# Kernel tuning notes

Hardware: AMD Instinct MI355X
Metric: run time of the kernel (lower is better)

The kernel has to match this reference:

```python
import jax, jax.numpy as jnp
import numpy as np


def setup_inputs() -> dict:
    key = jax.random.key(0)
    k1, k2 = jax.random.split(key)
    N, H, K, E = 8192, 4096, 2, 64
    x = jax.random.normal(k1, (N, H), dtype=jnp.float32)
    row_idx = jnp.arange(N * K, dtype=jnp.int32).reshape(N, K)
    expert_idx = jax.random.randint(k2, (N, K), 0, E, dtype=jnp.int32)
    return {"x": x, "row_idx": row_idx, "expert_idx": expert_idx, "active_num": N * K}


def reference(x, row_idx, expert_idx, active_num):
    # x: [N, H]; row_idx, expert_idx: [N, K]
    N, H = x.shape
    K = expert_idx.shape[1]
    NK = N * K

    expert_flat = expert_idx.reshape(-1)  # [N*K]
    row_flat = row_idx.reshape(-1)        # [N*K]

    # Step 1: stable sort by expert id, carry row indices
    sorted_indices = jnp.argsort(expert_flat, stable=True)
    expanded_expert_idx = expert_flat[sorted_indices]
    dst_to_src = row_flat[sorted_indices]

    # Step 2: invert the permutation: src_to_dst[dst_to_src[i]] = i
    expanded_row_idx = jnp.zeros(NK, dtype=jnp.int32).at[dst_to_src].set(
        jnp.arange(NK, dtype=jnp.int32)
    )

    # Step 3: gather x rows; dst_to_src % N gives the original token row
    expanded_x = x[dst_to_src % N]  # [N*K, H]

    return expanded_x, expanded_row_idx, expanded_expert_idx
```

## Files before the change

kernel.cpp:

```cpp
#include <hip/hip_runtime.h>
#include <hip/hip_bf16.h>

#define TPB 256
#define NEXPERT 64

typedef float f32x4 __attribute__((ext_vector_type(4)));

__global__ void k_hist(const int* __restrict__ expert, int NK, int NB,
                       int* __restrict__ counts) {
    __shared__ int h[NEXPERT];
    const int b = blockIdx.x;
    for (int e = threadIdx.x; e < NEXPERT; e += blockDim.x) h[e] = 0;
    __syncthreads();
    const int i = b * TPB + threadIdx.x;
    if (i < NK) atomicAdd(&h[expert[i]], 1);
    __syncthreads();
    for (int e = threadIdx.x; e < NEXPERT; e += blockDim.x)
        counts[e * NB + b] = h[e];
}

__global__ void k_scan(int* __restrict__ counts, int M) {
    __shared__ int s[1024];
    const int t = threadIdx.x;
    const int nt = blockDim.x;
    const int ipt = (M + nt - 1) / nt;
    int v[8];
    int sum = 0;
    for (int j = 0; j < ipt; ++j) {
        const int idx = t * ipt + j;
        v[j] = (idx < M) ? counts[idx] : 0;
        sum += v[j];
    }
    s[t] = sum;
    __syncthreads();
    for (int off = 1; off < nt; off <<= 1) {
        const int x = (t >= off) ? s[t - off] : 0;
        __syncthreads();
        s[t] += x;
        __syncthreads();
    }
    int base = (t == 0) ? 0 : s[t - 1];
    for (int j = 0; j < ipt; ++j) {
        const int idx = t * ipt + j;
        const int c = v[j];
        if (idx < M) counts[idx] = base;
        base += c;
    }
}

__global__ void k_scatter(const int* __restrict__ expert,
                          const int* __restrict__ rowi,
                          int NK, int NB,
                          const int* __restrict__ base,
                          float* __restrict__ out_row,
                          float* __restrict__ out_expert,
                          int* __restrict__ dst_of_r) {
    __shared__ int h[TPB / 64][NEXPERT + 1];
    const int b = blockIdx.x;
    const int tid = threadIdx.x;
    const int w = tid >> 6;
    const int lane = tid & 63;
    const int i = b * TPB + tid;
    const bool valid = (i < NK);
    const int e = valid ? expert[i] : NEXPERT;

    for (int idx = tid; idx < (TPB / 64) * (NEXPERT + 1); idx += TPB)
        (&h[0][0])[idx] = 0;
    __syncthreads();

    unsigned long long mask = ~0ull;
#pragma unroll
    for (int bit = 0; bit < 7; ++bit) {
        const unsigned long long bv = __ballot((e >> bit) & 1);
        mask &= ((e >> bit) & 1) ? bv : ~bv;
    }
    const int rank_w = __popcll(mask & ((1ull << lane) - 1ull));
    const int cnt_w  = __popcll(mask);
    if (rank_w == 0) h[w][e] = cnt_w;
    __syncthreads();

    if (valid) {
        int rank = rank_w;
        for (int w2 = 0; w2 < w; ++w2) rank += h[w2][e];
        const int dst = base[e * NB + b] + rank;
        const int r = rowi[i];
        out_expert[dst] = (float)e;
        out_row[r] = (float)dst;
        dst_of_r[r] = dst;
    }
}

template <int K>
__global__ void k_gatherT(const float* __restrict__ x,
                          const int* __restrict__ dst_of_r,
                          float* __restrict__ out_x, int H, int N) {
    const int t = blockIdx.x;
    const f32x4* __restrict__ src = (const f32x4*)(x + (size_t)t * (size_t)H);
    size_t ob[K];
#pragma unroll
    for (int kk = 0; kk < K; ++kk)
        ob[kk] = (size_t)dst_of_r[t + kk * N] * (size_t)H;
    const int n4 = H >> 2;
    for (int j = threadIdx.x; j < n4; j += blockDim.x) {
        const f32x4 v = src[j];
#pragma unroll
        for (int kk = 0; kk < K; ++kk)
            __builtin_nontemporal_store(v, (f32x4*)(out_x + ob[kk]) + j);
    }
}

__global__ void k_gather_gen(const float* __restrict__ x,
                             const int* __restrict__ dst_of_r,
                             float* __restrict__ out_x, int H, int N, int K) {
    const int t = blockIdx.x;
    const f32x4* __restrict__ src = (const f32x4*)(x + (size_t)t * (size_t)H);
    const int n4 = H >> 2;
    for (int kk = 0; kk < K; ++kk) {
        const size_t ob = (size_t)dst_of_r[t + kk * N] * (size_t)H;
        for (int j = threadIdx.x; j < n4; j += blockDim.x)
            __builtin_nontemporal_store(src[j], (f32x4*)(out_x + ob) + j);
    }
}

extern "C" void kernel_launch(void* const* d_in, const int* in_sizes, int n_in,
                              void* d_out, int out_size, void* d_ws, size_t ws_size,
                              hipStream_t stream) {
    const float* x    = (const float*)d_in[0];
    const int*   rowi = (const int*)d_in[1];
    const int*   expi = (const int*)d_in[2];

    const int NK = in_sizes[1];
    const int H  = (out_size - 2 * NK) / NK;
    const int N  = in_sizes[0] / H;
    const int K  = NK / N;
    const int NB = (NK + TPB - 1) / TPB;

    float* out_x      = (float*)d_out;
    float* out_row    = out_x + (size_t)NK * (size_t)H;
    float* out_expert = out_row + NK;

    int* counts   = (int*)d_ws;
    int* dst_of_r = counts + NEXPERT * NB;

    k_hist   <<<NB, TPB, 0, stream>>>(expi, NK, NB, counts);
    k_scan   <<<1, 1024, 0, stream>>>(counts, NEXPERT * NB);
    k_scatter<<<NB, TPB, 0, stream>>>(expi, rowi, NK, NB, counts,
                                      out_row, out_expert, dst_of_r);

    switch (K) {
        case 1: k_gatherT<1><<<N, TPB, 0, stream>>>(x, dst_of_r, out_x, H, N); break;
        case 2: k_gatherT<2><<<N, TPB, 0, stream>>>(x, dst_of_r, out_x, H, N); break;
        case 3: k_gatherT<3><<<N, TPB, 0, stream>>>(x, dst_of_r, out_x, H, N); break;
        case 4: k_gatherT<4><<<N, TPB, 0, stream>>>(x, dst_of_r, out_x, H, N); break;
        default: k_gather_gen<<<N, TPB, 0, stream>>>(x, dst_of_r, out_x, H, N, K); break;
    }
}
```

Before: 77.08 us.

## Fuse histogram, scan and scatter into a single-block prelude kernel

Replaces the three-kernel counting sort (per-block histogram, global scan, scatter) with one 1024-thread single-block kernel. It computes expert counts via wave ballots, scans them with shuffles, then ranks and scatters in chunks. The gather kernel reads destination indices from the float row output instead of a separate int workspace. This removes two launches and workspace traffic, but serializes the sort onto one CU with many block barriers.

Result: slower. 100.9 us (+30.9%).

```diff
diff --git a/kernel.cpp b/kernel.cpp
--- a/kernel.cpp
+++ b/kernel.cpp
@@ -3,103 +3,99 @@
 
 #define TPB 256
 #define NEXPERT 64
+#define PRE_T 1024
+#define PRE_W (PRE_T / 64)
 
 typedef float f32x4 __attribute__((ext_vector_type(4)));
 
-__global__ void k_hist(const int* __restrict__ expert, int NK, int NB,
-                       int* __restrict__ counts) {
-    __shared__ int h[NEXPERT];
-    const int b = blockIdx.x;
-    for (int e = threadIdx.x; e < NEXPERT; e += blockDim.x) h[e] = 0;
-    __syncthreads();
-    const int i = b * TPB + threadIdx.x;
-    if (i < NK) atomicAdd(&h[expert[i]], 1);
-    __syncthreads();
-    for (int e = threadIdx.x; e < NEXPERT; e += blockDim.x)
-        counts[e * NB + b] = h[e];
-}
-
-__global__ void k_scan(int* __restrict__ counts, int M) {
-    __shared__ int s[1024];
-    const int t = threadIdx.x;
-    const int nt = blockDim.x;
-    const int ipt = (M + nt - 1) / nt;
-    int v[8];
-    int sum = 0;
-    for (int j = 0; j < ipt; ++j) {
-        const int idx = t * ipt + j;
-        v[j] = (idx < M) ? counts[idx] : 0;
-        sum += v[j];
-    }
-    s[t] = sum;
-    __syncthreads();
-    for (int off = 1; off < nt; off <<= 1) {
-        const int x = (t >= off) ? s[t - off] : 0;
-        __syncthreads();
-        s[t] += x;
-        __syncthreads();
-    }
-    int base = (t == 0) ? 0 : s[t - 1];
-    for (int j = 0; j < ipt; ++j) {
-        const int idx = t * ipt + j;
-        const int c = v[j];
-        if (idx < M) counts[idx] = base;
-        base += c;
-    }
-}
-
-__global__ void k_scatter(const int* __restrict__ expert,
-                          const int* __restrict__ rowi,
-                          int NK, int NB,
-                          const int* __restrict__ base,
-                          float* __restrict__ out_row,
-                          float* __restrict__ out_expert,
-                          int* __restrict__ dst_of_r) {
-    __shared__ int h[TPB / 64][NEXPERT + 1];
-    const int b = blockIdx.x;
+__global__ __launch_bounds__(PRE_T) void k_prelude(
+    const int* __restrict__ expert, const int* __restrict__ rowi, int NK,
+    float* __restrict__ out_row, float* __restrict__ out_expert) {
+    __shared__ int hist[NEXPERT];
+    __shared__ int wcnt[PRE_W][NEXPERT + 1];
     const int tid = threadIdx.x;
     const int w = tid >> 6;
     const int lane = tid & 63;
-    const int i = b * TPB + tid;
-    const bool valid = (i < NK);
-    const int e = valid ? expert[i] : NEXPERT;
 
-    for (int idx = tid; idx < (TPB / 64) * (NEXPERT + 1); idx += TPB)
-        (&h[0][0])[idx] = 0;
+    for (int idx = tid; idx < NEXPERT; idx += PRE_T) hist[idx] = 0;
     __syncthreads();
 
-    unsigned long long mask = ~0ull;
+    for (int base_i = 0; base_i < NK; base_i += PRE_T) {
+        const int i = base_i + tid;
+        const bool valid = (i < NK);
+        const int e = valid ? expert[i] : NEXPERT;
+        unsigned long long mask = ~0ull;
 #pragma unroll
-    for (int bit = 0; bit < 7; ++bit) {
-        const unsigned long long bv = __ballot((e >> bit) & 1);
-        mask &= ((e >> bit) & 1) ? bv : ~bv;
+        for (int bit = 0; bit < 7; ++bit) {
+            const unsigned long long bv = __ballot((e >> bit) & 1);
+            mask &= ((e >> bit) & 1) ? bv : ~bv;
+        }
+        const int rank_w = __popcll(mask & ((1ull << lane) - 1ull));
+        if (valid && rank_w == 0) atomicAdd(&hist[e], __popcll(mask));
     }
-    const int rank_w = __popcll(mask & ((1ull << lane) - 1ull));
-    const int cnt_w  = __popcll(mask);
-    if (rank_w == 0) h[w][e] = cnt_w;
     __syncthreads();
 
-    if (valid) {
-        int rank = rank_w;
-        for (int w2 = 0; w2 < w; ++w2) rank += h[w2][e];
-        const int dst = base[e * NB + b] + rank;
-        const int r = rowi[i];
-        out_expert[dst] = (float)e;
-        out_row[r] = (float)dst;
-        dst_of_r[r] = dst;
+    if (tid < NEXPERT) {
+        const int c = hist[tid];
+        int v = c;
+#pragma unroll
+        for (int off = 1; off < NEXPERT; off <<= 1) {
+            const int u = __shfl_up(v, off, 64);
+            if (lane >= off) v += u;
+        }
+        hist[tid] = v - c;
+    }
+    __syncthreads();
+
+    for (int base_i = 0; base_i < NK; base_i += PRE_T) {
+        const int i = base_i + tid;
+        const bool valid = (i < NK);
+        const int e = valid ? expert[i] : NEXPERT;
+
+        for (int idx = tid; idx < PRE_W * (NEXPERT + 1); idx += PRE_T)
+            (&wcnt[0][0])[idx] = 0;
+        __syncthreads();
+
+        unsigned long long mask = ~0ull;
+#pragma unroll
+        for (int bit = 0; bit < 7; ++bit) {
+            const unsigned long long bv = __ballot((e >> bit) & 1);
+            mask &= ((e >> bit) & 1) ? bv : ~bv;
+        }
+        const int rank_w = __popcll(mask & ((1ull << lane) - 1ull));
+        const int cnt_w  = __popcll(mask);
+        if (valid && rank_w == 0) wcnt[w][e] = cnt_w;
+        __syncthreads();
+
+        if (valid) {
+            int rank = rank_w;
+            for (int w2 = 0; w2 < w; ++w2) rank += wcnt[w2][e];
+            const int dst = hist[e] + rank;
+            const int r = rowi[i];
+            out_row[r] = (float)dst;
+            out_expert[dst] = (float)e;
+        }
+        __syncthreads();
+
+        if (tid < NEXPERT) {
+            int tot = 0;
+            for (int w2 = 0; w2 < PRE_W; ++w2) tot += wcnt[w2][tid];
+            hist[tid] += tot;
+        }
+        __syncthreads();
     }
 }
 
 template <int K>
 __global__ void k_gatherT(const float* __restrict__ x,
-                          const int* __restrict__ dst_of_r,
+                          const float* __restrict__ row_f,
                           float* __restrict__ out_x, int H, int N) {
     const int t = blockIdx.x;
     const f32x4* __restrict__ src = (const f32x4*)(x + (size_t)t * (size_t)H);
     size_t ob[K];
 #pragma unroll
     for (int kk = 0; kk < K; ++kk)
-        ob[kk] = (size_t)dst_of_r[t + kk * N] * (size_t)H;
+        ob[kk] = (size_t)(int)row_f[t + kk * N] * (size_t)H;
     const int n4 = H >> 2;
     for (int j = threadIdx.x; j < n4; j += blockDim.x) {
         const f32x4 v = src[j];
@@ -110,13 +106,13 @@
 }
 
 __global__ void k_gather_gen(const float* __restrict__ x,
-                             const int* __restrict__ dst_of_r,
+                             const float* __restrict__ row_f,
                              float* __restrict__ out_x, int H, int N, int K) {
     const int t = blockIdx.x;
     const f32x4* __restrict__ src = (const f32x4*)(x + (size_t)t * (size_t)H);
     const int n4 = H >> 2;
     for (int kk = 0; kk < K; ++kk) {
-        const size_t ob = (size_t)dst_of_r[t + kk * N] * (size_t)H;
+        const size_t ob = (size_t)(int)row_f[t + kk * N] * (size_t)H;
         for (int j = threadIdx.x; j < n4; j += blockDim.x)
             __builtin_nontemporal_store(src[j], (f32x4*)(out_x + ob) + j);
     }
@@ -133,25 +129,18 @@
     const int H  = (out_size - 2 * NK) / NK;
     const int N  = in_sizes[0] / H;
     const int K  = NK / N;
-    const int NB = (NK + TPB - 1) / TPB;
 
     float* out_x      = (float*)d_out;
     float* out_row    = out_x + (size_t)NK * (size_t)H;
     float* out_expert = out_row + NK;
 
-    int* counts   = (int*)d_ws;
-    int* dst_of_r = counts + NEXPERT * NB;
-
-    k_hist   <<<NB, TPB, 0, stream>>>(expi, NK, NB, counts);
-    k_scan   <<<1, 1024, 0, stream>>>(counts, NEXPERT * NB);
-    k_scatter<<<NB, TPB, 0, stream>>>(expi, rowi, NK, NB, counts,
-                                      out_row, out_expert, dst_of_r);
+    k_prelude<<<1, PRE_T, 0, stream>>>(expi, rowi, NK, out_row, out_expert);
 
     switch (K) {
-        case 1: k_gatherT<1><<<N, TPB, 0, stream>>>(x, dst_of_r, out_x, H, N); break;
-        case 2: k_gatherT<2><<<N, TPB, 0, stream>>>(x, dst_of_r, out_x, H, N); break;
-        case 3: k_gatherT<3><<<N, TPB, 0, stream>>>(x, dst_of_r, out_x, H, N); break;
-        case 4: k_gatherT<4><<<N, TPB, 0, stream>>>(x, dst_of_r, out_x, H, N); break;
-        default: k_gather_gen<<<N, TPB, 0, stream>>>(x, dst_of_r, out_x, H, N, K); break;
+        case 1: k_gatherT<1><<<N, TPB, 0, stream>>>(x, out_row, out_x, H, N); break;
+        case 2: k_gatherT<2><<<N, TPB, 0, stream>>>(x, out_row, out_x, H, N); break;
+        case 3: k_gatherT<3><<<N, TPB, 0, stream>>>(x, out_row, out_x, H, N); break;
+        case 4: k_gatherT<4><<<N, TPB, 0, stream>>>(x, out_row, out_x, H, N); break;
+        default: k_gather_gen<<<N, TPB, 0, stream>>>(x, out_row, out_x, H, N, K); break;
     }
 }
```
